# Optimization experiments

Measured on AMD Instinct MI355X. Metric: run time of the kernel, lower is better.

## Reference

```python
import jax, jax.numpy as jnp
import numpy as np

N = 50000        # num nodes (hyperedge ids also live in [0, N), matching old PyG quirk)
E = 1600000      # num incidence pairs
F_IN = 512       # input features
HEADS = 8
OUT1 = 8         # hconv1 out_channels per head
HID = HEADS * OUT1  # 64
NCLS = 7
NEG_SLOPE = 0.2


def setup_inputs() -> dict:
    key = jax.random.key(0)
    ks = jax.random.split(key, 8)
    x = jax.random.normal(ks[0], (N, F_IN), dtype=jnp.float32)
    edge_index = jax.random.randint(ks[1], (2, E), 0, N, dtype=jnp.int32)
    hyperedge_weight = jax.random.uniform(ks[2], (N,), dtype=jnp.float32) + 0.1
    W1 = jax.random.normal(ks[3], (F_IN, HEADS * OUT1), dtype=jnp.float32) * (1.0 / np.sqrt(F_IN))
    att1 = jax.random.normal(ks[4], (1, HEADS, 2 * OUT1), dtype=jnp.float32) * 0.1
    b1 = jnp.zeros((HEADS * OUT1,), dtype=jnp.float32)
    W2 = jax.random.normal(ks[5], (HID, NCLS), dtype=jnp.float32) * (1.0 / np.sqrt(HID))
    b2 = jnp.zeros((NCLS,), dtype=jnp.float32)
    return {"x": x, "edge_index": edge_index, "hyperedge_weight": hyperedge_weight,
            "W1": W1, "att1": att1, "b1": b1, "W2": W2, "b2": b2}


def _segment_softmax(a, seg, n):
    # numerically-stable softmax over groups defined by seg (per column / head)
    amax = jax.ops.segment_max(a, seg, num_segments=n)
    amax = jnp.where(jnp.isfinite(amax), amax, 0.0)
    ex = jnp.exp(a - amax[seg])
    den = jax.ops.segment_sum(ex, seg, num_segments=n)
    return ex / (den[seg] + 1e-16)


def _hconv(x, edge_index, hw, W, bias, heads, out_ch, att=None):
    """Old-PyG HypergraphConv forward (dropout disabled / eval mode)."""
    row, col = edge_index[0], edge_index[1]   # row: node ids, col: hyperedge ids
    n = x.shape[0]
    ones = jnp.ones(row.shape[0], dtype=x.dtype)
    xh = (x @ W).reshape(n, heads, out_ch)    # [N, H, C]

    if att is not None:
        # split att to avoid materializing cat([x_i, x_j]) per edge
        s_i = (xh * att[..., :out_ch]).sum(-1)   # [N, H]
        s_j = (xh * att[..., out_ch:]).sum(-1)   # [N, H]
        a = jax.nn.leaky_relu(s_i[row] + s_j[col], NEG_SLOPE)  # [E, H]
        alpha = _segment_softmax(a, row, n)      # grouped by source node
    else:
        alpha = None

    # node degree norm D (weighted by hyperedge weight)
    D = jax.ops.segment_sum(hw[col], row, num_segments=n)
    Dinv = jnp.where(D > 0, 1.0 / D, 0.0)
    # hyperedge degree norm B, scaled by hyperedge weight
    Bdeg = jax.ops.segment_sum(ones, col, num_segments=n)
    Binv = jnp.where(Bdeg > 0, 1.0 / Bdeg, 0.0) * hw

    # propagate 1: nodes -> hyperedges, norm = B[target]
    msg1 = xh[row] * Binv[col][:, None, None]          # [E, H, C]
    if alpha is not None:
        msg1 = msg1 * alpha[:, :, None]
    out_e = jax.ops.segment_sum(msg1, col, num_segments=n)  # [N, H, C]

    # propagate 2: hyperedges -> nodes, norm = D[target]
    msg2 = out_e[col] * Dinv[row][:, None, None]       # [E, H, C]
    if alpha is not None:
        msg2 = msg2 * alpha[:, :, None]
    out = jax.ops.segment_sum(msg2, row, num_segments=n)    # [N, H, C]

    return out.reshape(n, heads * out_ch) + bias   # concat=True


def reference(x, edge_index, hyperedge_weight, W1, att1, b1, W2, b2):
    # eval mode: F.dropout(p=0.6) is identity
    h = jax.nn.elu(_hconv(x, edge_index, hyperedge_weight, W1, b1, HEADS, OUT1, att1))
    out = _hconv(h, edge_index, hyperedge_weight, W2, b2, 1, NCLS, None)
    return jax.nn.log_softmax(out, axis=1)
```

## Files before the change

kernel.cpp:

```cpp
#include <hip/hip_runtime.h>
#include <hip/hip_bf16.h>
#include <cmath>

#define NN    50000
#define EE    1600000
#define FIN   512
#define NHEAD 8
#define OUT1  8
#define HID   64
#define NCLS  7

#define NB    391
#define EPB   4096
#define LOG2E 1.4426950408889634f

#define OFF_XH     0
#define OFF_SJ     3200000
#define OFF_SIRD   3600000
#define OFF_DINV   4400000
#define OFF_BINV   4450000
#define OFF_ACCE   4500000
#define OFF_H      7700000
#define OFF_XH2    10900000
#define OFF_ACCE2  11300000
#define OFF_RPTR   11700000
#define OFF_CPTR   11760000
#define OFF_BHR    11820000
#define OFF_BHC    11821000
#define OFF_BSR    11822000
#define OFF_BSC    11823000
#define OFF_BCR    11824000
#define OFF_BCC    11825000
#define OFF_CSRRC  11830000
#define OFF_CSRCR  13430000

#define LRELU(a) ((a) > 0.f ? (a) : 0.2f * (a))

__device__ __forceinline__ float fexp2(float x) {
#if __has_builtin(__builtin_amdgcn_exp2f)
  return __builtin_amdgcn_exp2f(x);
#else
  return exp2f(x);
#endif
}

__global__ __launch_bounds__(512) void zero_small(int* __restrict__ bh_r,
                                                  int* __restrict__ bh_c) {
  int t = threadIdx.x;
  if (t <= NB) { bh_r[t] = 0; bh_c[t] = 0; }
}

__global__ __launch_bounds__(256) void bucket_hist(const int* __restrict__ ei,
                                                   int* __restrict__ bh_r,
                                                   int* __restrict__ bh_c) {
  __shared__ int hr[NB], hc[NB];
  int t = threadIdx.x;
  for (int i = t; i < NB; i += 256) { hr[i] = 0; hc[i] = 0; }
  __syncthreads();
  for (int i = blockIdx.x * 256 + t; i < EE; i += gridDim.x * 256) {
    atomicAdd(hr + (ei[i] >> 7), 1);
    atomicAdd(hc + (ei[EE + i] >> 7), 1);
  }
  __syncthreads();
  for (int i = t; i < NB; i += 256) {
    if (hr[i]) atomicAdd(bh_r + i, hr[i]);
    if (hc[i]) atomicAdd(bh_c + i, hc[i]);
  }
}

__global__ __launch_bounds__(512) void bucket_scan(const int* __restrict__ bh_r,
                                                   const int* __restrict__ bh_c,
                                                   int* __restrict__ bs_r,
                                                   int* __restrict__ bs_c,
                                                   int* __restrict__ bc_r,
                                                   int* __restrict__ bc_c) {
  __shared__ int lds[512];
  int t = threadIdx.x;
  for (int side = 0; side < 2; ++side) {
    const int* bh = side ? bh_c : bh_r;
    int* bs = side ? bs_c : bs_r;
    int* bc = side ? bc_c : bc_r;
    int v = (t < NB) ? bh[t] : 0;
    lds[t] = v;
    __syncthreads();
    for (int off = 1; off < 512; off <<= 1) {
      int u = (t >= off) ? lds[t - off] : 0;
      __syncthreads();
      lds[t] += u;
      __syncthreads();
    }
    int excl = lds[t] - v;
    if (t <= NB) bs[t] = excl;
    if (t < NB) bc[t] = excl;
    __syncthreads();
  }
}

__global__ __launch_bounds__(256) void phaseA(const int* __restrict__ ei,
                                              int* __restrict__ bc_r,
                                              int* __restrict__ bc_c,
                                              int* __restrict__ tmp_r,
                                              int* __restrict__ tmp_c) {
  __shared__ int er[EPB];
  __shared__ int ec[EPB];
  __shared__ int hr[NB], hc[NB];
  const int e0 = blockIdx.x * EPB;
  const int cntE = min(EPB, EE - e0);
  const int t = threadIdx.x;
  for (int i = t; i < cntE; i += 256) { er[i] = ei[e0 + i]; ec[i] = ei[EE + e0 + i]; }
  for (int i = t; i < NB; i += 256) { hr[i] = 0; hc[i] = 0; }
  __syncthreads();
  for (int i = t; i < cntE; i += 256) {
    atomicAdd(hr + (er[i] >> 7), 1);
    atomicAdd(hc + (ec[i] >> 7), 1);
  }
  __syncthreads();
  for (int i = t; i < NB; i += 256) {
    int n = hr[i];
    hr[i] = n ? atomicAdd(bc_r + i, n) : 0;
    n = hc[i];
    hc[i] = n ? atomicAdd(bc_c + i, n) : 0;
  }
  __syncthreads();
  for (int i = t; i < cntE; i += 256) {
    int r = er[i], c = ec[i];
    int pr = atomicAdd(hr + (r >> 7), 1);
    tmp_r[pr] = ((r & 127) << 16) | c;
    int pc = atomicAdd(hc + (c >> 7), 1);
    tmp_c[pc] = ((c & 127) << 16) | r;
  }
}

__global__ __launch_bounds__(256) void phaseB(const int* __restrict__ tmp_r,
                                              const int* __restrict__ tmp_c,
                                              const int* __restrict__ bs_r,
                                              const int* __restrict__ bs_c,
                                              const float* __restrict__ hw,
                                              int* __restrict__ rptr,
                                              int* __restrict__ cptr,
                                              int* __restrict__ csr_row_c,
                                              int* __restrict__ csr_col_r,
                                              float* __restrict__ Binv) {
  const int side = blockIdx.x >= NB ? 1 : 0;
  const int b = blockIdx.x - side * NB;
  const int* tmp = side ? tmp_c : tmp_r;
  const int* bs = side ? bs_c : bs_r;
  int* ptr = side ? cptr : rptr;
  int* csr = side ? csr_col_r : csr_row_c;

  const int base = bs[b];
  const int M = bs[b + 1] - base;
  __shared__ int cnt[128], pre[128], cur[128];
  const int t = threadIdx.x;
  if (t < 128) cnt[t] = 0;
  __syncthreads();
  for (int i = t; i < M; i += 256) atomicAdd(cnt + (tmp[base + i] >> 16), 1);
  __syncthreads();
  if (t < 128) pre[t] = cnt[t];
  __syncthreads();
  for (int off = 1; off < 128; off <<= 1) {
    int u = (t >= off && t < 128) ? pre[t - off] : 0;
    __syncthreads();
    if (t < 128) pre[t] += u;
    __syncthreads();
  }
  const int node0 = b << 7;
  if (t < 128) {
    int excl = pre[t] - cnt[t];
    int g = node0 + t;
    if (g <= NN) ptr[g] = base + excl;
    cur[t] = base + excl;
    if (side && g < NN) Binv[g] = cnt[t] > 0 ? hw[g] / (float)cnt[t] : 0.f;
  }
  __syncthreads();
  for (int i = t; i < M; i += 256) {
    int e = tmp[base + i];
    int pos = atomicAdd(cur + (e >> 16), 1);
    csr[pos] = e & 0xFFFF;
  }
}

__global__ __launch_bounds__(256) void gemm1_kernel(const float* __restrict__ x,
                                                    const float* __restrict__ W1,
                                                    float* __restrict__ p0,
                                                    float* __restrict__ p1) {
  __shared__ float lx[32][66];
  __shared__ float lw[32][68];
  const int t = threadIdx.x;
  const int row0 = blockIdx.x * 64;
  const int kbase = blockIdx.y * (FIN / 2);
  float* __restrict__ dst = blockIdx.y ? p1 : p0;
  const int ty = t >> 4, tx = t & 15;
  const int r0 = ty * 4, c0 = tx * 4;
  const int sr = t >> 2;
  const int sk = (t & 3) * 8;
  const int grow = row0 + sr;
  const int wk = t >> 3;
  const int wc = (t & 7) * 8;

  float acc[4][4] = {};

  for (int kb = kbase; kb < kbase + FIN / 2; kb += 32) {
    {
      float4 a0 = make_float4(0.f, 0.f, 0.f, 0.f), a1 = a0;
      if (grow < NN) {
        const float4* p = reinterpret_cast<const float4*>(x + (size_t)grow * FIN + kb + sk);
        a0 = p[0]; a1 = p[1];
      }
      lx[sk + 0][sr] = a0.x; lx[sk + 1][sr] = a0.y;
      lx[sk + 2][sr] = a0.z; lx[sk + 3][sr] = a0.w;
      lx[sk + 4][sr] = a1.x; lx[sk + 5][sr] = a1.y;
      lx[sk + 6][sr] = a1.z; lx[sk + 7][sr] = a1.w;
    }
    {
      const float4* q = reinterpret_cast<const float4*>(W1 + (size_t)(kb + wk) * HID + wc);
      float4 b0 = q[0], b1v = q[1];
      *reinterpret_cast<float4*>(&lw[wk][wc]) = b0;
      *reinterpret_cast<float4*>(&lw[wk][wc + 4]) = b1v;
    }
    __syncthreads();
#pragma unroll
    for (int kk = 0; kk < 32; ++kk) {
      const float4 af = *reinterpret_cast<const float4*>(&lx[kk][r0]);
      const float4 bf = *reinterpret_cast<const float4*>(&lw[kk][c0]);
      const float a4[4] = {af.x, af.y, af.z, af.w};
      const float b4[4] = {bf.x, bf.y, bf.z, bf.w};
#pragma unroll
      for (int i = 0; i < 4; ++i)
#pragma unroll
        for (int j = 0; j < 4; ++j)
          acc[i][j] = fmaf(a4[i], b4[j], acc[i][j]);
    }
    __syncthreads();
  }
#pragma unroll
  for (int i = 0; i < 4; ++i) {
    int gr = row0 + r0 + i;
    if (gr < NN) {
      float4 v = make_float4(acc[i][0], acc[i][1], acc[i][2], acc[i][3]);
      *reinterpret_cast<float4*>(dst + (size_t)gr * HID + c0) = v;
    }
  }
}

__global__ __launch_bounds__(256) void attscore_kernel(float* __restrict__ xh,
                                                       const float* __restrict__ p1,
                                                       const float* __restrict__ att1,
                                                       float2* __restrict__ sird,
                                                       float* __restrict__ s_j) {
  int t = blockIdx.x * 256 + threadIdx.x;
  if (t >= NN * NHEAD) return;
  int hh = t & 7;
  const size_t base = (size_t)t * 8;
  float4 a0 = *reinterpret_cast<const float4*>(xh + base);
  float4 a1 = *reinterpret_cast<const float4*>(xh + base + 4);
  float4 q0 = *reinterpret_cast<const float4*>(p1 + base);
  float4 q1 = *reinterpret_cast<const float4*>(p1 + base + 4);
  float v[8] = {a0.x + q0.x, a0.y + q0.y, a0.z + q0.z, a0.w + q0.w,
                a1.x + q1.x, a1.y + q1.y, a1.z + q1.z, a1.w + q1.w};
  float si = 0.f, sj = 0.f;
#pragma unroll
  for (int c = 0; c < OUT1; ++c) {
    si = fmaf(v[c], att1[hh * 16 + c], si);
    sj = fmaf(v[c], att1[hh * 16 + 8 + c], sj);
  }
  *reinterpret_cast<float4*>(xh + base)     = make_float4(v[0], v[1], v[2], v[3]);
  *reinterpret_cast<float4*>(xh + base + 4) = make_float4(v[4], v[5], v[6], v[7]);
  sird[t] = make_float2(si * LOG2E, 0.f);
  s_j[t] = sj * LOG2E;
}

__global__ __launch_bounds__(256) void den_csr(const int* __restrict__ rptr,
                                               const int* __restrict__ csr_row_c,
                                               const float* __restrict__ s_j,
                                               const float* __restrict__ hw,
                                               float2* __restrict__ sird,
                                               float* __restrict__ dinv) {
  int wid = (blockIdx.x * 256 + threadIdx.x) >> 6;
  int lane = threadIdx.x & 63;
  if (wid >= NN) return;
  int r = wid;
  int hh = lane & 7;
  int eslot = lane >> 3;
  float si = sird[r * 8 + hh].x;
  int beg = rptr[r], end = rptr[r + 1];
  float aexp = 0.f, ad = 0.f;
  int i = beg + eslot;
  for (; i + 8 < end; i += 16) {
    int c0 = csr_row_c[i], c1 = csr_row_c[i + 8];
    float sj0 = s_j[c0 * 8 + hh], sj1 = s_j[c1 * 8 + hh];
    float h0 = hw[c0], h1 = hw[c1];
    float a0 = LRELU(si + sj0), a1 = LRELU(si + sj1);
    aexp += fexp2(a0) + fexp2(a1);
    ad += h0 + h1;
  }
  if (i < end) {
    int c = csr_row_c[i];
    float a = LRELU(si + s_j[c * 8 + hh]);
    aexp += fexp2(a);
    ad += hw[c];
  }
  aexp += __shfl_xor(aexp, 8);
  aexp += __shfl_xor(aexp, 16);
  aexp += __shfl_xor(aexp, 32);
  ad += __shfl_xor(ad, 8);
  ad += __shfl_xor(ad, 16);
  ad += __shfl_xor(ad, 32);
  if (eslot == 0) {
    reinterpret_cast<float*>(sird)[(r * 8 + hh) * 2 + 1] = 1.0f / (aexp + 1e-16f);
    if (hh == 0) dinv[r] = ad > 0.f ? 1.0f / ad : 0.f;
  }
}

__global__ __launch_bounds__(256) void prop1_csr(const int* __restrict__ cptr,
                                                 const int* __restrict__ csr_col_r,
                                                 const float* __restrict__ xh,
                                                 const float2* __restrict__ sird,
                                                 const float* __restrict__ s_j,
                                                 const float* __restrict__ Binv,
                                                 float* __restrict__ acc_e) {
  int wid = (blockIdx.x * 256 + threadIdx.x) >> 6;
  int lane = threadIdx.x & 63;
  if (wid >= NN) return;
  const int c = wid;
  const int hh = lane >> 3;
  const int j = lane & 7;
  const int abase = lane & 56;
  float sj = s_j[c * 8 + hh];
  int beg = cptr[c], end = cptr[c + 1];
  float acc = 0.f;
  int i = beg;
  for (; i + 8 <= end; i += 8) {
    int rj = csr_col_r[i + j];
    float2 q = sird[rj * 8 + hh];
    float a = LRELU(q.x + sj);
    float aexp = fexp2(a) * q.y;
#pragma unroll
    for (int j2 = 0; j2 < 8; ++j2) {
      int r = __shfl(rj, j2);
      float al = __shfl(aexp, abase + j2);
      acc = fmaf(xh[(r << 6) + lane], al, acc);
    }
  }
  for (; i < end; ++i) {
    int r = csr_col_r[i];
    float2 q = sird[r * 8 + hh];
    float a = LRELU(q.x + sj);
    acc = fmaf(xh[(r << 6) + lane], fexp2(a) * q.y, acc);
  }
  acc_e[(c << 6) + lane] = acc * Binv[c];
}

__global__ __launch_bounds__(256) void prop2_csr(const int* __restrict__ rptr,
                                                 const int* __restrict__ csr_row_c,
                                                 const float* __restrict__ acc_e,
                                                 const float2* __restrict__ sird,
                                                 const float* __restrict__ s_j,
                                                 const float* __restrict__ dinv,
                                                 const float* __restrict__ b1,
                                                 float* __restrict__ h) {
  int wid = (blockIdx.x * 256 + threadIdx.x) >> 6;
  int lane = threadIdx.x & 63;
  if (wid >= NN) return;
  const int r = wid;
  const int hh = lane >> 3;
  const int j = lane & 7;
  const int abase = lane & 56;
  float2 sr = sird[r * 8 + hh];
  const float si = sr.x, rd = sr.y;
  int beg = rptr[r], end = rptr[r + 1];
  float acc = 0.f;
  int i = beg;
  for (; i + 8 <= end; i += 8) {
    int cj = csr_row_c[i + j];
    float sjv = s_j[cj * 8 + hh];
    float aexp = fexp2(LRELU(si + sjv));
#pragma unroll
    for (int j2 = 0; j2 < 8; ++j2) {
      int cc = __shfl(cj, j2);
      float al = __shfl(aexp, abase + j2);
      acc = fmaf(acc_e[(cc << 6) + lane], al, acc);
    }
  }
  for (; i < end; ++i) {
    int cc = csr_row_c[i];
    float aexp = fexp2(LRELU(si + s_j[cc * 8 + hh]));
    acc = fmaf(acc_e[(cc << 6) + lane], aexp, acc);
  }
  acc *= rd;
  float v = fmaf(acc, dinv[r], b1[lane]);
  h[(r << 6) + lane] = v > 0.f ? v : expm1f(v);
}

__global__ __launch_bounds__(256) void gemm2_kernel(const float* __restrict__ h,
                                                    const float* __restrict__ W2,
                                                    float* __restrict__ xh2) {
  int t = blockIdx.x * 256 + threadIdx.x;
  if (t >= NN * 8) return;
  int n = t >> 3, k = t & 7;
  if (k == 7) { xh2[t] = 0.f; return; }
  const float* hp = h + (size_t)n * HID;
  float acc = 0.f;
#pragma unroll
  for (int c = 0; c < HID; ++c) acc = fmaf(hp[c], W2[c * NCLS + k], acc);
  xh2[t] = acc;
}

__global__ __launch_bounds__(256) void prop3_csr(const int* __restrict__ cptr,
                                                 const int* __restrict__ csr_col_r,
                                                 const float* __restrict__ xh2,
                                                 const float* __restrict__ Binv,
                                                 float* __restrict__ acc_e2) {
  int t = blockIdx.x * 256 + threadIdx.x;
  int g = t >> 3, k = t & 7;
  if (g >= NN) return;
  int beg = cptr[g], end = cptr[g + 1];
  float acc = 0.f;
  int i = beg;
  for (; i + 3 < end; i += 4) {
    int r0 = csr_col_r[i], r1 = csr_col_r[i + 1];
    int r2 = csr_col_r[i + 2], r3 = csr_col_r[i + 3];
    float v0 = xh2[r0 * 8 + k], v1 = xh2[r1 * 8 + k];
    float v2 = xh2[r2 * 8 + k], v3 = xh2[r3 * 8 + k];
    acc += (v0 + v1) + (v2 + v3);
  }
  for (; i < end; ++i) acc += xh2[csr_col_r[i] * 8 + k];
  acc_e2[g * 8 + k] = acc * Binv[g];
}

__global__ __launch_bounds__(256) void prop4_csr(const int* __restrict__ rptr,
                                                 const int* __restrict__ csr_row_c,
                                                 const float* __restrict__ acc_e2,
                                                 const float* __restrict__ dinv,
                                                 const float* __restrict__ b2,
                                                 float* __restrict__ out) {
  int t = blockIdx.x * 256 + threadIdx.x;
  int r = t >> 3, k = t & 7;
  if (r >= NN) return;
  int beg = rptr[r], end = rptr[r + 1];
  float acc = 0.f;
  int i = beg;
  for (; i + 3 < end; i += 4) {
    int c0 = csr_row_c[i], c1 = csr_row_c[i + 1];
    int c2 = csr_row_c[i + 2], c3 = csr_row_c[i + 3];
    float v0 = acc_e2[c0 * 8 + k], v1 = acc_e2[c1 * 8 + k];
    float v2 = acc_e2[c2 * 8 + k], v3 = acc_e2[c3 * 8 + k];
    acc += (v0 + v1) + (v2 + v3);
  }
  for (; i < end; ++i) acc += acc_e2[csr_row_c[i] * 8 + k];
  float v = (k < NCLS) ? fmaf(acc, dinv[r], b2[k]) : -INFINITY;
  float m = v;
  m = fmaxf(m, __shfl_xor(m, 1, 8));
  m = fmaxf(m, __shfl_xor(m, 2, 8));
  m = fmaxf(m, __shfl_xor(m, 4, 8));
  float ex = (k < NCLS) ? expf(v - m) : 0.f;
  float s = ex;
  s += __shfl_xor(s, 1, 8);
  s += __shfl_xor(s, 2, 8);
  s += __shfl_xor(s, 4, 8);
  float lse = m + logf(s);
  if (k < NCLS) out[(size_t)r * NCLS + k] = v - lse;
}

extern "C" void kernel_launch(void* const* d_in, const int* in_sizes, int n_in,
                              void* d_out, int out_size, void* d_ws, size_t ws_size,
                              hipStream_t stream) {
  const float* x    = (const float*)d_in[0];
  const int*   ei   = (const int*)d_in[1];
  const float* hw   = (const float*)d_in[2];
  const float* W1   = (const float*)d_in[3];
  const float* att1 = (const float*)d_in[4];
  const float* b1   = (const float*)d_in[5];
  const float* W2   = (const float*)d_in[6];
  const float* b2   = (const float*)d_in[7];
  float* out = (float*)d_out;
  float* ws  = (float*)d_ws;

  float* xh     = ws + OFF_XH;
  float* s_j    = ws + OFF_SJ;
  float2* sird  = (float2*)(ws + OFF_SIRD);
  float* dinv   = ws + OFF_DINV;
  float* Binv   = ws + OFF_BINV;
  float* acc_e  = ws + OFF_ACCE;
  float* hbuf   = ws + OFF_H;
  float* xh2    = ws + OFF_XH2;
  float* acc_e2 = ws + OFF_ACCE2;
  int* rptr = (int*)(ws + OFF_RPTR);
  int* cptr = (int*)(ws + OFF_CPTR);
  int* bh_r = (int*)(ws + OFF_BHR);
  int* bh_c = (int*)(ws + OFF_BHC);
  int* bs_r = (int*)(ws + OFF_BSR);
  int* bs_c = (int*)(ws + OFF_BSC);
  int* bc_r = (int*)(ws + OFF_BCR);
  int* bc_c = (int*)(ws + OFF_BCC);
  int* csr_row_c = (int*)(ws + OFF_CSRRC);
  int* csr_col_r = (int*)(ws + OFF_CSRCR);
  int* tmp_r = (int*)(ws + OFF_XH);
  int* tmp_c = (int*)(ws + OFF_ACCE);

  zero_small<<<1, 512, 0, stream>>>(bh_r, bh_c);
  bucket_hist<<<256, 256, 0, stream>>>(ei, bh_r, bh_c);
  bucket_scan<<<1, 512, 0, stream>>>(bh_r, bh_c, bs_r, bs_c, bc_r, bc_c);
  phaseA<<<(EE + EPB - 1) / EPB, 256, 0, stream>>>(ei, bc_r, bc_c, tmp_r, tmp_c);
  phaseB<<<2 * NB, 256, 0, stream>>>(tmp_r, tmp_c, bs_r, bs_c, hw,
                                     rptr, cptr, csr_row_c, csr_col_r, Binv);

  {
    dim3 g((NN + 63) / 64, 2);
    gemm1_kernel<<<g, 256, 0, stream>>>(x, W1, xh, hbuf);
  }
  attscore_kernel<<<(NN * NHEAD + 255) / 256, 256, 0, stream>>>(xh, hbuf, att1, sird, s_j);
  den_csr<<<(NN * 64 + 255) / 256, 256, 0, stream>>>(rptr, csr_row_c, s_j, hw, sird, dinv);
  prop1_csr<<<(NN * 64 + 255) / 256, 256, 0, stream>>>(cptr, csr_col_r, xh, sird, s_j, Binv, acc_e);
  prop2_csr<<<(NN * 64 + 255) / 256, 256, 0, stream>>>(rptr, csr_row_c, acc_e, sird, s_j,
                                                       dinv, b1, hbuf);

  gemm2_kernel<<<(NN * 8 + 255) / 256, 256, 0, stream>>>(hbuf, W2, xh2);
  prop3_csr<<<(NN * 8 + 255) / 256, 256, 0, stream>>>(cptr, csr_col_r, xh2, Binv, acc_e2);
  prop4_csr<<<(NN * 8 + 255) / 256, 256, 0, stream>>>(rptr, csr_row_c, acc_e2, dinv, b2, out);
}
```

Baseline: 348.5 us.

## Split layer-1 propagation into four head-pair passes over blocked feature layout

Attention-score kernel now writes xh in a head-pair-blocked layout (4 slabs of N×16). Propagation 1 and 2 each run as four passes, one per pair of heads, so every gathered slab is 3.2 MB and more likely to stay cache-resident during random gathers. Inside each pass a wave handles 4 edges in parallel with 16 channels and reduces with shuffles. This adds 6 extra launches and recomputes the attention exponentials once per pass, and each gathered row is now only 64 bytes.

```diff
diff --git a/kernel.cpp b/kernel.cpp
--- a/kernel.cpp
+++ b/kernel.cpp
@@ -13,13 +13,14 @@
 #define NB    391
 #define EPB   4096
 #define LOG2E 1.4426950408889634f
-
-#define OFF_XH     0
+#define NPASS 4
+
+#define OFF_P0     0
 #define OFF_SJ     3200000
 #define OFF_SIRD   3600000
 #define OFF_DINV   4400000
 #define OFF_BINV   4450000
-#define OFF_ACCE   4500000
+#define OFF_XHB    4500000
 #define OFF_H      7700000
 #define OFF_XH2    10900000
 #define OFF_ACCE2  11300000
@@ -243,17 +244,18 @@
   }
 }
 
-__global__ __launch_bounds__(256) void attscore_kernel(float* __restrict__ xh,
+__global__ __launch_bounds__(256) void attscore_kernel(const float* __restrict__ p0,
                                                        const float* __restrict__ p1,
                                                        const float* __restrict__ att1,
+                                                       float* __restrict__ xhb,
                                                        float2* __restrict__ sird,
                                                        float* __restrict__ s_j) {
   int t = blockIdx.x * 256 + threadIdx.x;
   if (t >= NN * NHEAD) return;
-  int hh = t & 7;
+  int n = t >> 3, hh = t & 7;
   const size_t base = (size_t)t * 8;
-  float4 a0 = *reinterpret_cast<const float4*>(xh + base);
-  float4 a1 = *reinterpret_cast<const float4*>(xh + base + 4);
+  float4 a0 = *reinterpret_cast<const float4*>(p0 + base);
+  float4 a1 = *reinterpret_cast<const float4*>(p0 + base + 4);
   float4 q0 = *reinterpret_cast<const float4*>(p1 + base);
   float4 q1 = *reinterpret_cast<const float4*>(p1 + base + 4);
   float v[8] = {a0.x + q0.x, a0.y + q0.y, a0.z + q0.z, a0.w + q0.w,
@@ -264,8 +266,9 @@
     si = fmaf(v[c], att1[hh * 16 + c], si);
     sj = fmaf(v[c], att1[hh * 16 + 8 + c], sj);
   }
-  *reinterpret_cast<float4*>(xh + base)     = make_float4(v[0], v[1], v[2], v[3]);
-  *reinterpret_cast<float4*>(xh + base + 4) = make_float4(v[4], v[5], v[6], v[7]);
+  float* dst = xhb + ((size_t)(hh >> 1) * NN + n) * 16 + (hh & 1) * 8;
+  *reinterpret_cast<float4*>(dst)     = make_float4(v[0], v[1], v[2], v[3]);
+  *reinterpret_cast<float4*>(dst + 4) = make_float4(v[4], v[5], v[6], v[7]);
   sird[t] = make_float2(si * LOG2E, 0.f);
   s_j[t] = sj * LOG2E;
 }
@@ -312,84 +315,101 @@
   }
 }
 
-__global__ __launch_bounds__(256) void prop1_csr(const int* __restrict__ cptr,
-                                                 const int* __restrict__ csr_col_r,
-                                                 const float* __restrict__ xh,
-                                                 const float2* __restrict__ sird,
-                                                 const float* __restrict__ s_j,
-                                                 const float* __restrict__ Binv,
-                                                 float* __restrict__ acc_e) {
+__global__ __launch_bounds__(256) void prop1_split(const int* __restrict__ cptr,
+                                                   const int* __restrict__ csr_col_r,
+                                                   const float* __restrict__ xhp,
+                                                   const float2* __restrict__ sird,
+                                                   const float* __restrict__ s_j,
+                                                   const float* __restrict__ Binv,
+                                                   float* __restrict__ acc_ep,
+                                                   int p) {
   int wid = (blockIdx.x * 256 + threadIdx.x) >> 6;
   int lane = threadIdx.x & 63;
   if (wid >= NN) return;
   const int c = wid;
-  const int hh = lane >> 3;
-  const int j = lane & 7;
-  const int abase = lane & 56;
-  float sj = s_j[c * 8 + hh];
+  const int g = lane >> 4;
+  const int ch = lane & 15;
+  const int head = 2 * p + (ch >> 3);
+  const float sj = s_j[c * 8 + head];
   int beg = cptr[c], end = cptr[c + 1];
   float acc = 0.f;
   int i = beg;
   for (; i + 8 <= end; i += 8) {
-    int rj = csr_col_r[i + j];
-    float2 q = sird[rj * 8 + hh];
-    float a = LRELU(q.x + sj);
-    float aexp = fexp2(a) * q.y;
-#pragma unroll
-    for (int j2 = 0; j2 < 8; ++j2) {
-      int r = __shfl(rj, j2);
-      float al = __shfl(aexp, abase + j2);
-      acc = fmaf(xh[(r << 6) + lane], al, acc);
-    }
-  }
-  for (; i < end; ++i) {
-    int r = csr_col_r[i];
-    float2 q = sird[r * 8 + hh];
-    float a = LRELU(q.x + sj);
-    acc = fmaf(xh[(r << 6) + lane], fexp2(a) * q.y, acc);
-  }
-  acc_e[(c << 6) + lane] = acc * Binv[c];
-}
-
-__global__ __launch_bounds__(256) void prop2_csr(const int* __restrict__ rptr,
-                                                 const int* __restrict__ csr_row_c,
-                                                 const float* __restrict__ acc_e,
-                                                 const float2* __restrict__ sird,
-                                                 const float* __restrict__ s_j,
-                                                 const float* __restrict__ dinv,
-                                                 const float* __restrict__ b1,
-                                                 float* __restrict__ h) {
+    int r0 = csr_col_r[i + g];
+    int r1 = csr_col_r[i + 4 + g];
+    float2 q0 = sird[r0 * 8 + head];
+    float2 q1 = sird[r1 * 8 + head];
+    float v0 = xhp[(r0 << 4) + ch];
+    float v1 = xhp[(r1 << 4) + ch];
+    float al0 = fexp2(LRELU(q0.x + sj)) * q0.y;
+    float al1 = fexp2(LRELU(q1.x + sj)) * q1.y;
+    acc = fmaf(v0, al0, acc);
+    acc = fmaf(v1, al1, acc);
+  }
+  for (; i + 4 <= end; i += 4) {
+    int r = csr_col_r[i + g];
+    float2 q = sird[r * 8 + head];
+    float v = xhp[(r << 4) + ch];
+    acc = fmaf(v, fexp2(LRELU(q.x + sj)) * q.y, acc);
+  }
+  if (i + g < end) {
+    int r = csr_col_r[i + g];
+    float2 q = sird[r * 8 + head];
+    float v = xhp[(r << 4) + ch];
+    acc = fmaf(v, fexp2(LRELU(q.x + sj)) * q.y, acc);
+  }
+  acc += __shfl_xor(acc, 16);
+  acc += __shfl_xor(acc, 32);
+  if (g == 0) acc_ep[(c << 4) + ch] = acc * Binv[c];
+}
+
+__global__ __launch_bounds__(256) void prop2_split(const int* __restrict__ rptr,
+                                                   const int* __restrict__ csr_row_c,
+                                                   const float* __restrict__ acc_ep,
+                                                   const float2* __restrict__ sird,
+                                                   const float* __restrict__ s_j,
+                                                   const float* __restrict__ dinv,
+                                                   const float* __restrict__ b1,
+                                                   float* __restrict__ h,
+                                                   int p) {
   int wid = (blockIdx.x * 256 + threadIdx.x) >> 6;
   int lane = threadIdx.x & 63;
   if (wid >= NN) return;
   const int r = wid;
-  const int hh = lane >> 3;
-  const int j = lane & 7;
-  const int abase = lane & 56;
-  float2 sr = sird[r * 8 + hh];
+  const int g = lane >> 4;
+  const int ch = lane & 15;
+  const int head = 2 * p + (ch >> 3);
+  float2 sr = sird[r * 8 + head];
   const float si = sr.x, rd = sr.y;
   int beg = rptr[r], end = rptr[r + 1];
   float acc = 0.f;
   int i = beg;
   for (; i + 8 <= end; i += 8) {
-    int cj = csr_row_c[i + j];
-    float sjv = s_j[cj * 8 + hh];
-    float aexp = fexp2(LRELU(si + sjv));
-#pragma unroll
-    for (int j2 = 0; j2 < 8; ++j2) {
-      int cc = __shfl(cj, j2);
-      float al = __shfl(aexp, abase + j2);
-      acc = fmaf(acc_e[(cc << 6) + lane], al, acc);
-    }
-  }
-  for (; i < end; ++i) {
-    int cc = csr_row_c[i];
-    float aexp = fexp2(LRELU(si + s_j[cc * 8 + hh]));
-    acc = fmaf(acc_e[(cc << 6) + lane], aexp, acc);
-  }
-  acc *= rd;
-  float v = fmaf(acc, dinv[r], b1[lane]);
-  h[(r << 6) + lane] = v > 0.f ? v : expm1f(v);
+    int c0 = csr_row_c[i + g];
+    int c1 = csr_row_c[i + 4 + g];
+    float sj0 = s_j[c0 * 8 + head];
+    float sj1 = s_j[c1 * 8 + head];
+    float v0 = acc_ep[(c0 << 4) + ch];
+    float v1 = acc_ep[(c1 << 4) + ch];
+    acc = fmaf(v0, fexp2(LRELU(si + sj0)), acc);
+    acc = fmaf(v1, fexp2(LRELU(si + sj1)), acc);
+  }
+  for (; i + 4 <= end; i += 4) {
+    int cc = csr_row_c[i + g];
+    float v = acc_ep[(cc << 4) + ch];
+    acc = fmaf(v, fexp2(LRELU(si + s_j[cc * 8 + head])), acc);
+  }
+  if (i + g < end) {
+    int cc = csr_row_c[i + g];
+    float v = acc_ep[(cc << 4) + ch];
+    acc = fmaf(v, fexp2(LRELU(si + s_j[cc * 8 + head])), acc);
+  }
+  acc += __shfl_xor(acc, 16);
+  acc += __shfl_xor(acc, 32);
+  if (g == 0) {
+    float val = fmaf(acc * rd, dinv[r], b1[16 * p + ch]);
+    h[(r << 6) + 16 * p + ch] = val > 0.f ? val : expm1f(val);
+  }
 }
 
 __global__ __launch_bounds__(256) void gemm2_kernel(const float* __restrict__ h,
@@ -476,12 +496,12 @@
   float* out = (float*)d_out;
   float* ws  = (float*)d_ws;
 
-  float* xh     = ws + OFF_XH;
+  float* p0buf  = ws + OFF_P0;
   float* s_j    = ws + OFF_SJ;
   float2* sird  = (float2*)(ws + OFF_SIRD);
   float* dinv   = ws + OFF_DINV;
   float* Binv   = ws + OFF_BINV;
-  float* acc_e  = ws + OFF_ACCE;
+  float* xhb    = ws + OFF_XHB;
   float* hbuf   = ws + OFF_H;
   float* xh2    = ws + OFF_XH2;
   float* acc_e2 = ws + OFF_ACCE2;
@@ -495,8 +515,8 @@
   int* bc_c = (int*)(ws + OFF_BCC);
   int* csr_row_c = (int*)(ws + OFF_CSRRC);
   int* csr_col_r = (int*)(ws + OFF_CSRCR);
-  int* tmp_r = (int*)(ws + OFF_XH);
-  int* tmp_c = (int*)(ws + OFF_ACCE);
+  int* tmp_r = (int*)(ws + OFF_P0);
+  int* tmp_c = (int*)(ws + OFF_XHB);
 
   zero_small<<<1, 512, 0, stream>>>(bh_r, bh_c);
   bucket_hist<<<256, 256, 0, stream>>>(ei, bh_r, bh_c);
@@ -507,13 +527,23 @@
 
   {
     dim3 g((NN + 63) / 64, 2);
-    gemm1_kernel<<<g, 256, 0, stream>>>(x, W1, xh, hbuf);
-  }
-  attscore_kernel<<<(NN * NHEAD + 255) / 256, 256, 0, stream>>>(xh, hbuf, att1, sird, s_j);
+    gemm1_kernel<<<g, 256, 0, stream>>>(x, W1, p0buf, hbuf);
+  }
+  attscore_kernel<<<(NN * NHEAD + 255) / 256, 256, 0, stream>>>(p0buf, hbuf, att1,
+                                                                xhb, sird, s_j);
   den_csr<<<(NN * 64 + 255) / 256, 256, 0, stream>>>(rptr, csr_row_c, s_j, hw, sird, dinv);
-  prop1_csr<<<(NN * 64 + 255) / 256, 256, 0, stream>>>(cptr, csr_col_r, xh, sird, s_j, Binv, acc_e);
-  prop2_csr<<<(NN * 64 + 255) / 256, 256, 0, stream>>>(rptr, csr_row_c, acc_e, sird, s_j,
-                                                       dinv, b1, hbuf);
+
+  const int pgrid = (NN * 64 + 255) / 256;
+  float* acc_eb = p0buf;
+  for (int p = 0; p < NPASS; ++p)
+    prop1_split<<<pgrid, 256, 0, stream>>>(cptr, csr_col_r,
+                                           xhb + (size_t)p * NN * 16,
+                                           sird, s_j, Binv,
+                                           acc_eb + (size_t)p * NN * 16, p);
+  for (int p = 0; p < NPASS; ++p)
+    prop2_split<<<pgrid, 256, 0, stream>>>(rptr, csr_row_c,
+                                           acc_eb + (size_t)p * NN * 16,
+                                           sird, s_j, dinv, b1, hbuf, p);
 
   gemm2_kernel<<<(NN * 8 + 255) / 256, 256, 0, stream>>>(hbuf, W2, xh2);
   prop3_csr<<<(NN * 8 + 255) / 256, 256, 0, stream>>>(cptr, csr_col_r, xh2, Binv, acc_e2);
```

New measurement: 502.1 us. +44.1%, slower.
